# Performance work log

Hardware: AMD Instinct MI355X
Metric: run time of the kernel (lower is better)

The kernel has to match this reference:

```python
import jax, jax.numpy as jnp
import numpy as np

B, S, D = 2, 2048, 1024
H, DH = 16, 64  # num_heads, attention_dim


def setup_inputs() -> dict:
    key = jax.random.key(0)
    ks = jax.random.split(key, 10)
    x = jax.random.normal(ks[0], (B, S, D), dtype=jnp.float32)
    # causal mask, broadcast over batch and heads (mask==0 -> -inf)
    mask = jnp.tril(jnp.ones((S, S), dtype=jnp.int32))[None, None]
    s = 1.0 / np.sqrt(D)
    Wq = jax.random.normal(ks[1], (D, H * DH), dtype=jnp.float32) * s
    bq = jnp.zeros((H * DH,), dtype=jnp.float32)
    Wk = jax.random.normal(ks[2], (D, H * DH), dtype=jnp.float32) * s
    bk = jnp.zeros((H * DH,), dtype=jnp.float32)
    Wv = jax.random.normal(ks[3], (D, H * DH), dtype=jnp.float32) * s
    bv = jnp.zeros((H * DH,), dtype=jnp.float32)
    Wo = jax.random.normal(ks[4], (H * DH, D), dtype=jnp.float32) * (1.0 / np.sqrt(H * DH))
    bo = jnp.zeros((D,), dtype=jnp.float32)
    return {"x": x, "mask": mask, "Wq": Wq, "bq": bq, "Wk": Wk, "bk": bk,
            "Wv": Wv, "bv": bv, "Wo": Wo, "bo": bo}


def reference(x, mask, Wq, bq, Wk, bk, Wv, bv, Wo, bo):
    b, s, _ = x.shape
    q = (x @ Wq + bq).reshape(b, s, H, DH)
    k = (x @ Wk + bk).reshape(b, s, H, DH)
    v = (x @ Wv + bv).reshape(b, s, H, DH)
    # scores: [B, H, S, S]
    scores = jnp.einsum("bshd,bthd->bhst", q, k) / jnp.sqrt(jnp.float32(DH))
    scores = jnp.where(mask == 0, -jnp.inf, scores)
    w = jax.nn.softmax(scores, axis=-1)
    attended = jnp.einsum("bhst,bthd->bshd", w, v).reshape(b, s, H * DH)
    return attended @ Wo + bo
```

## Files before the change

### kernel.cpp

```cpp
#include <hip/hip_runtime.h>
#include <hip/hip_bf16.h>

#define B_ 2
#define S_ 2048
#define D_ 1024
#define H_ 16
#define DH_ 64

typedef __attribute__((ext_vector_type(8))) short bf16x8;
typedef __attribute__((ext_vector_type(4))) float f32x4;

#define QSCALE 0.18033688011112042f

__device__ __forceinline__ ushort f2b(float f){
  __hip_bfloat16 h = __float2bfloat16(f);
  return *reinterpret_cast<ushort*>(&h);
}

__device__ __forceinline__ unsigned cvtpk(float lo, float hi){
  unsigned r;
  asm("v_cvt_pk_bf16_f32 %0, %1, %2" : "=v"(r) : "v"(lo), "v"(hi));
  return r;
}

__device__ __forceinline__ void gload16(const ushort* g, ushort* l){
  __builtin_amdgcn_global_load_lds((const __attribute__((address_space(1))) unsigned*)g,
                                   (__attribute__((address_space(3))) unsigned*)l, 16, 0, 0);
}

__global__ __launch_bounds__(256) void k_prep(const float* __restrict__ x, ushort* __restrict__ xb,
                                              const float* __restrict__ Wq, const float* __restrict__ Wk,
                                              const float* __restrict__ Wv, const float* __restrict__ Wo,
                                              ushort* __restrict__ WqkvT, ushort* __restrict__ WoT){
  int bid = blockIdx.x, tid = threadIdx.x;
  if (bid < 2048){
    int i = (bid*256 + tid)*8;
    float4 v0 = *(const float4*)(x + i);
    float4 v1 = *(const float4*)(x + i + 4);
    uint4 o;
    o.x = f2b(v0.x) | ((unsigned)f2b(v0.y)<<16);
    o.y = f2b(v0.z) | ((unsigned)f2b(v0.w)<<16);
    o.z = f2b(v1.x) | ((unsigned)f2b(v1.y)<<16);
    o.w = f2b(v1.z) | ((unsigned)f2b(v1.w)<<16);
    *(uint4*)(xb + i) = o;
    return;
  }
  bid -= 2048;
  const int w = bid >> 10, tb = bid & 1023;
  const float* src = (w==0)?Wq:(w==1)?Wk:(w==2)?Wv:Wo;
  ushort* dst = (w==3)?WoT : WqkvT + (size_t)w*(1024*1024);
  __shared__ float tile[32][33];
  const int bx2 = tb & 31, by2 = tb >> 5;
  const int c0 = bx2*32, r0 = by2*32;
  const int tx = tid & 31, ty = tid >> 5;
  #pragma unroll
  for (int i=0;i<4;i++)
    tile[ty + i*8][tx] = src[(size_t)(r0 + ty + i*8)*1024 + c0 + tx];
  __syncthreads();
  #pragma unroll
  for (int i=0;i<4;i++)
    dst[(size_t)(c0 + ty + i*8)*1024 + r0 + tx] = f2b(tile[tx][ty + i*8]);
}

__global__ __launch_bounds__(512, 4) void k_gemm_qkv(const ushort* __restrict__ A,
                                                     const ushort* __restrict__ BT,
                                                     const float* __restrict__ b0p,
                                                     const float* __restrict__ b1p,
                                                     const float* __restrict__ b2p,
                                                     ushort* __restrict__ Cp,
                                                     int M, int N, int K){
  __shared__ ushort As[256*64];
  __shared__ ushort Bs[128*64];
  const int tid = threadIdx.x;
  const int nbn = N >> 7;
  const int bm = blockIdx.x / nbn, bn = blockIdx.x % nbn;
  const int m0 = bm << 8, n0 = bn << 7;
  const int wave = tid >> 6, lane = tid & 63;
  const int wm = (wave >> 1) << 6, wn = (wave & 1) << 6;
  const int lr = lane & 15, lq = lane >> 4;

  f32x4 acc[4][4] = {};

  const int r0 = tid >> 3;
  const int gk = (tid & 7) ^ (r0 & 7);
  const ushort* Agb = A  + (size_t)(m0 + r0)*K + gk*8;
  const ushort* Bgb = BT + (size_t)(n0 + r0)*K + gk*8;
  const int lofs = tid*8;

  for (int kt = 0; kt < K; kt += 64){
    __syncthreads();
    #pragma unroll
    for (int j=0;j<4;j++)
      gload16(Agb + (size_t)j*64*K + kt, &As[lofs + j*4096]);
    #pragma unroll
    for (int j=0;j<2;j++)
      gload16(Bgb + (size_t)j*64*K + kt, &Bs[lofs + j*4096]);
    __syncthreads();
    #pragma unroll
    for (int kk=0;kk<2;kk++){
      bf16x8 af[4], bfr[4];
      #pragma unroll
      for (int i=0;i<4;i++){
        int ra = wm + i*16 + lr;
        af[i]  = *(bf16x8*)&As[ra*64 + (((kk*4+lq) ^ (ra & 7)) << 3)];
        int rb = wn + i*16 + lr;
        bfr[i] = *(bf16x8*)&Bs[rb*64 + (((kk*4+lq) ^ (rb & 7)) << 3)];
      }
      __builtin_amdgcn_s_setprio(1);
      #pragma unroll
      for (int mi=0;mi<4;mi++)
        #pragma unroll
        for (int ni=0;ni<4;ni++)
          acc[mi][ni] = __builtin_amdgcn_mfma_f32_16x16x32_bf16(af[mi], bfr[ni], acc[mi][ni], 0, 0, 0);
      __builtin_amdgcn_s_setprio(0);
    }
  }

  const int seg = n0 >> 10;
  const float* bp = (seg==0 ? b0p : (seg==1 ? b1p : b2p));
  #pragma unroll
  for (int mi=0;mi<4;mi++){
    #pragma unroll
    for (int ni=0;ni<4;ni++){
      int col = n0 + wn + ni*16 + lr;
      int cl = col & 1023;
      float bv = bp[cl];
      int row0 = m0 + wm + mi*16 + lq*4;
      ushort* Qb = Cp;
      if (seg == 0){
        #pragma unroll
        for (int r=0;r<4;r++)
          Qb[(size_t)(row0+r)*1024 + cl] = f2b((acc[mi][ni][r] + bv) * QSCALE);
      } else if (seg == 1){
        ushort* Kb = Qb + (4u<<20);
        #pragma unroll
        for (int r=0;r<4;r++)
          Kb[(size_t)(row0+r)*1024 + cl] = f2b(acc[mi][ni][r] + bv);
      } else {
        ushort* Vt = Qb + (8u<<20);
        int bb = row0 >> 11, srow = row0 & 2047;
        uint2 pk;
        pk.x = cvtpk(acc[mi][ni][0]+bv, acc[mi][ni][1]+bv);
        pk.y = cvtpk(acc[mi][ni][2]+bv, acc[mi][ni][3]+bv);
        *(uint2*)&Vt[((size_t)(bb*1024 + cl))*2048 + srow] = pk;
      }
    }
  }
}

__global__ __launch_bounds__(256) void k_gemm_out(const ushort* __restrict__ A,
                                                  const ushort* __restrict__ BT,
                                                  const float* __restrict__ bias,
                                                  float* __restrict__ Cp,
                                                  int M, int N, int K){
  __shared__ ushort As[128*64];
  __shared__ ushort Bs[128*64];
  const int tid = threadIdx.x;
  const int nbn = N >> 7;
  const int bm = blockIdx.x / nbn, bn = blockIdx.x % nbn;
  const int m0 = bm << 7, n0 = bn << 7;
  const int wave = tid >> 6, lane = tid & 63;
  const int wm = (wave >> 1) << 6, wn = (wave & 1) << 6;
  const int lr = lane & 15, lq = lane >> 4;

  f32x4 acc[4][4] = {};

  const ushort* Ag[4]; const ushort* Bg[4]; int lofs[4];
  #pragma unroll
  for (int j=0;j<4;j++){
    int c = tid + j*256, row = c >> 3, slot = c & 7;
    int gk2 = slot ^ (row & 7);
    Ag[j] = A  + (size_t)(m0 + row)*K + gk2*8;
    Bg[j] = BT + (size_t)(n0 + row)*K + gk2*8;
    lofs[j] = c*8;
  }

  for (int kt = 0; kt < K; kt += 64){
    __syncthreads();
    #pragma unroll
    for (int j=0;j<4;j++){
      gload16(Ag[j] + kt, &As[lofs[j]]);
      gload16(Bg[j] + kt, &Bs[lofs[j]]);
    }
    __syncthreads();
    #pragma unroll
    for (int kk=0;kk<2;kk++){
      bf16x8 af[4], bfr[4];
      #pragma unroll
      for (int i=0;i<4;i++){
        int ra = wm + i*16 + lr;
        af[i]  = *(bf16x8*)&As[ra*64 + (((kk*4+lq) ^ (ra & 7)) << 3)];
        int rb = wn + i*16 + lr;
        bfr[i] = *(bf16x8*)&Bs[rb*64 + (((kk*4+lq) ^ (rb & 7)) << 3)];
      }
      __builtin_amdgcn_s_setprio(1);
      #pragma unroll
      for (int mi=0;mi<4;mi++)
        #pragma unroll
        for (int ni=0;ni<4;ni++)
          acc[mi][ni] = __builtin_amdgcn_mfma_f32_16x16x32_bf16(af[mi], bfr[ni], acc[mi][ni], 0, 0, 0);
      __builtin_amdgcn_s_setprio(0);
    }
  }

  #pragma unroll
  for (int mi=0;mi<4;mi++){
    #pragma unroll
    for (int ni=0;ni<4;ni++){
      int col = n0 + wn + ni*16 + lr;
      float bv = bias[col];
      int row0 = m0 + wm + mi*16 + lq*4;
      #pragma unroll
      for (int r=0;r<4;r++)
        Cp[(size_t)(row0+r)*N + col] = acc[mi][ni][r] + bv;
    }
  }
}

__device__ __forceinline__ bf16x8 lds_frag(const ushort* base, int row, int colbytes){
  return *(const bf16x8*)((const char*)base + row*128 + (colbytes ^ ((row & 7) << 4)));
}

__global__ __launch_bounds__(256) void k_attn_mfma(const ushort* __restrict__ Qb,
                                                   const ushort* __restrict__ Kb,
                                                   const ushort* __restrict__ Vtg,
                                                   ushort* __restrict__ Ob,
                                                   ushort* __restrict__ accPb,
                                                   float* __restrict__ lP){
  __shared__ ushort Ks[64*64];
  __shared__ ushort Vs[64*64];
  __shared__ ushort Ps[4][16*64];
  const int bid = blockIdx.x;
  int bh, qt, t0, NT, half; bool split;
  if (bid < 1024){
    int s = bid >> 5; bh = bid & 31;
    qt = 31 - (s >> 1); half = s & 1; split = true;
    if (half == 0){ t0 = 16; NT = qt; }
    else          { t0 = 0;  NT = 15; }
  } else {
    int s = bid - 1024; qt = 15 - (s >> 5); bh = s & 31;
    t0 = 0; NT = qt; half = 0; split = false;
  }
  const bool diag = (!split) || (half == 0);
  const int h = bh & 15, b = bh >> 4;
  const int q0 = qt << 6;
  const int tid = threadIdx.x;
  const int wq = tid >> 6, lane = tid & 63;
  const int ql = lane & 15, g = lane >> 4;

  bf16x8 Qf0, Qf1;
  {
    const ushort* qp = Qb + (size_t)(b*S_ + q0 + wq*16 + ql)*1024 + h*64 + g*8;
    Qf0 = *(const bf16x8*)(qp);
    Qf1 = *(const bf16x8*)(qp + 32);
  }
  bf16x8 ones;
  #pragma unroll
  for (int i=0;i<8;i++) ones[i] = (short)0x3F80;

  f32x4 lsum = {};
  f32x4 acc[4] = {};

  const int r0c = tid >> 3, cc = tid & 7;
  const int r1c = r0c + 32;
  const int ofs0 = r0c*128 + ((cc*16) ^ ((r0c & 7) << 4));
  const int ofs1 = r1c*128 + ((cc*16) ^ ((r1c & 7) << 4));
  const ushort* Kp0 = Kb  + (size_t)(b*S_ + r0c)*1024 + h*64 + cc*8;
  const ushort* Kp1 = Kb  + (size_t)(b*S_ + r1c)*1024 + h*64 + cc*8;
  const ushort* Vp0 = Vtg + (size_t)(bh*64 + r0c)*2048 + cc*8;
  const ushort* Vp1 = Vtg + (size_t)(bh*64 + r1c)*2048 + cc*8;

  uint4 ka, kc, va, vc;
  #define ALOAD(t) { \
    ka = *(const uint4*)(Kp0 + (size_t)(t)*65536); \
    kc = *(const uint4*)(Kp1 + (size_t)(t)*65536); \
    va = *(const uint4*)(Vp0 + (t)*64); \
    vc = *(const uint4*)(Vp1 + (t)*64); }

  char* Pb = (char*)Ps + wq*2048;

  ALOAD(t0);
  for (int kt = t0; ; ++kt){
    __syncthreads();
    *(uint4*)((char*)Ks + ofs0) = ka;
    *(uint4*)((char*)Ks + ofs1) = kc;
    *(uint4*)((char*)Vs + ofs0) = va;
    *(uint4*)((char*)Vs + ofs1) = vc;
    __syncthreads();
    if (kt < NT) ALOAD(kt+1);

    f32x4 sf[4] = {};
    __builtin_amdgcn_s_setprio(1);
    #pragma unroll
    for (int ki=0; ki<4; ++ki){
      bf16x8 kf = lds_frag(Ks, ki*16 + ql, g*16);
      sf[ki] = __builtin_amdgcn_mfma_f32_16x16x32_bf16(kf, Qf0, sf[ki], 0, 0, 0);
    }
    #pragma unroll
    for (int ki=0; ki<4; ++ki){
      bf16x8 kf = lds_frag(Ks, ki*16 + ql, 64 + g*16);
      sf[ki] = __builtin_amdgcn_mfma_f32_16x16x32_bf16(kf, Qf1, sf[ki], 0, 0, 0);
    }
    __builtin_amdgcn_s_setprio(0);

    float s[16];
    #pragma unroll
    for (int ki=0; ki<4; ++ki)
      #pragma unroll
      for (int r=0; r<4; ++r)
        s[ki*4+r] = sf[ki][r];
    if (diag && kt == NT){
      const int th = q0 + wq*16 + ql - NT*64;
      #pragma unroll
      for (int ki=0; ki<4; ++ki)
        #pragma unroll
        for (int r=0; r<4; ++r)
          if (ki*16 + g*4 + r > th) s[ki*4+r] = -1e30f;
    }
    #pragma unroll
    for (int i=0; i<16; ++i) s[i] = exp2f(s[i]);

    #pragma unroll
    for (int ki=0; ki<4; ++ki){
      uint2 uu;
      uu.x = cvtpk(s[ki*4+0], s[ki*4+1]);
      uu.y = cvtpk(s[ki*4+2], s[ki*4+3]);
      *(uint2*)(Pb + ql*128 + ((ki*32 + g*8) ^ ((ql & 7) << 4))) = uu;
    }

    __builtin_amdgcn_s_setprio(1);
    #pragma unroll
    for (int ks=0; ks<2; ++ks){
      bf16x8 pf = *(const bf16x8*)(Pb + ql*128 + ((ks*64 + g*16) ^ ((ql & 7) << 4)));
      #pragma unroll
      for (int ni=0; ni<4; ++ni){
        bf16x8 vf = lds_frag(Vs, ni*16 + ql, ks*64 + g*16);
        acc[ni] = __builtin_amdgcn_mfma_f32_16x16x32_bf16(pf, vf, acc[ni], 0, 0, 0);
      }
      lsum = __builtin_amdgcn_mfma_f32_16x16x32_bf16(pf, ones, lsum, 0, 0, 0);
    }
    __builtin_amdgcn_s_setprio(0);

    if (kt == NT) break;
  }
  #undef ALOAD

  if (!split){
    ushort* Op = Ob + (size_t)(b*S_ + q0 + wq*16)*1024 + h*64;
    #pragma unroll
    for (int r=0; r<4; ++r){
      float ir = 1.0f / lsum[r];
      #pragma unroll
      for (int ni=0; ni<4; ++ni)
        Op[(size_t)(g*4 + r)*1024 + ni*16 + ql] = f2b(acc[ni][r] * ir);
    }
  } else {
    const int slot = (qt - 16)*32 + bh;
    const int rbase = half*32768 + slot*64 + wq*16;
    #pragma unroll
    for (int r=0; r<4; ++r){
      const int tr = rbase + g*4 + r;
      float ir = 1.0f / lsum[r];
      #pragma unroll
      for (int ni=0; ni<4; ++ni)
        accPb[(size_t)tr*64 + ni*16 + ql] = f2b(acc[ni][r] * ir);
      if (ql == 0) lP[tr] = lsum[r];
    }
  }
}

__global__ __launch_bounds__(256) void k_combine(const ushort* __restrict__ accPb,
                                                 const float* __restrict__ lP,
                                                 ushort* __restrict__ Ob){
  const int slot = blockIdx.x;
  const int qt = 16 + (slot >> 5), bh = slot & 31;
  const int b = bh >> 4, h = bh & 15;
  const int row = threadIdx.x >> 2, dq = (threadIdx.x & 3) * 16;
  const int trA = slot*64 + row, trB = 32768 + slot*64 + row;
  float lA = lP[trA], lB = lP[trB];
  float inv = 1.0f / (lA + lB);
  float wA = lA * inv, wB = lB * inv;
  const ushort* pa = accPb + (size_t)trA*64 + dq;
  const ushort* pb = accPb + (size_t)trB*64 + dq;
  uint4 a0 = *(const uint4*)pa, a1 = *(const uint4*)(pa + 8);
  uint4 b0 = *(const uint4*)pb, b1 = *(const uint4*)(pb + 8);
  unsigned aw[8] = {a0.x,a0.y,a0.z,a0.w,a1.x,a1.y,a1.z,a1.w};
  unsigned bw[8] = {b0.x,b0.y,b0.z,b0.w,b1.x,b1.y,b1.z,b1.w};
  unsigned ow[8];
  #pragma unroll
  for (int e=0;e<8;e++){
    float alo = __uint_as_float(aw[e] << 16), ahi = __uint_as_float(aw[e] & 0xffff0000u);
    float blo = __uint_as_float(bw[e] << 16), bhi = __uint_as_float(bw[e] & 0xffff0000u);
    ow[e] = cvtpk(alo*wA + blo*wB, ahi*wA + bhi*wB);
  }
  ushort* op = Ob + (size_t)(b*S_ + qt*64 + row)*1024 + h*64 + dq;
  uint4 o0, o1;
  o0.x=ow[0]; o0.y=ow[1]; o0.z=ow[2]; o0.w=ow[3];
  o1.x=ow[4]; o1.y=ow[5]; o1.z=ow[6]; o1.w=ow[7];
  *(uint4*)(op)     = o0;
  *(uint4*)(op + 8) = o1;
}

extern "C" void kernel_launch(void* const* d_in, const int* in_sizes, int n_in,
                              void* d_out, int out_size, void* d_ws, size_t ws_size,
                              hipStream_t stream){
  const float* x  = (const float*)d_in[0];
  const float* Wq = (const float*)d_in[2];
  const float* bq = (const float*)d_in[3];
  const float* Wk = (const float*)d_in[4];
  const float* bk = (const float*)d_in[5];
  const float* Wv = (const float*)d_in[6];
  const float* bv = (const float*)d_in[7];
  const float* Wo = (const float*)d_in[8];
  const float* bo = (const float*)d_in[9];

  char* ws = (char*)d_ws;
  const size_t MB = 1024u*1024u;
  ushort* xb    = (ushort*)(ws + 0);
  ushort* WqkvT = (ushort*)(ws + 8*MB);
  ushort* WoT   = (ushort*)(ws + 14*MB);
  ushort* Qb    = (ushort*)(ws + 16*MB);
  ushort* Kb    = (ushort*)(ws + 24*MB);
  ushort* Vtg   = (ushort*)(ws + 32*MB);
  float*  lP    = (float*)(ws + 40*MB);
  ushort* attb  = xb;
  ushort* accPb = (ushort*)d_out;

  const int MN = B_*S_;

  k_prep<<<dim3(6144), dim3(256), 0, stream>>>(x, xb, Wq, Wk, Wv, Wo, WqkvT, WoT);

  k_gemm_qkv<<<dim3((MN/256)*(3072/128)), dim3(512), 0, stream>>>(xb, WqkvT, bq, bk, bv, Qb, MN, 3072, 1024);

  k_attn_mfma<<<dim3(1536), dim3(256), 0, stream>>>(Qb, Kb, Vtg, attb, accPb, lP);
  k_combine<<<dim3(512), dim3(256), 0, stream>>>(accPb, lP, attb);

  k_gemm_out<<<dim3((MN/128)*(1024/128)), dim3(256), 0, stream>>>(attb, WoT, bo, (float*)d_out, MN, 1024, 1024);
}
```

Baseline: 112.5 us.

## Split attention KV range into fixed ten-tile chunks with multi-way combine

The attention work split changes from a two-way split for the upper half of query tiles to chunks of at most ten KV tiles, giving 1 to 4 chunks per query tile and 2176 blocks. The combine kernel now merges a variable number of partial results per row, weighted by their row sums. The aim is to even out per-block work and shorten the tail of the causal attention launch. In exchange it adds more partial-result traffic and a larger combine pass.

Measured after the change: 113.1 us. No clear change (+0.5%).

```diff
diff --git a/kernel.cpp b/kernel.cpp
--- a/kernel.cpp
+++ b/kernel.cpp
@@ -11,6 +11,11 @@
 typedef __attribute__((ext_vector_type(4))) float f32x4;
 
 #define QSCALE 0.18033688011112042f
+
+__device__ __forceinline__ int chunk_off(int qt){
+  return (qt <= 19) ? 2*(qt-10) : (qt <= 29 ? 20 + 3*(qt-20) : 50 + 4*(qt-30));
+}
+#define CHUNKS_PER_BH 58
 
 __device__ __forceinline__ ushort f2b(float f){
   __hip_bfloat16 h = __float2bfloat16(f);
@@ -231,17 +236,17 @@
   __shared__ ushort Vs[64*64];
   __shared__ ushort Ps[4][16*64];
   const int bid = blockIdx.x;
-  int bh, qt, t0, NT, half; bool split;
-  if (bid < 1024){
-    int s = bid >> 5; bh = bid & 31;
-    qt = 31 - (s >> 1); half = s & 1; split = true;
-    if (half == 0){ t0 = 16; NT = qt; }
-    else          { t0 = 0;  NT = 15; }
-  } else {
-    int s = bid - 1024; qt = 15 - (s >> 5); bh = s & 31;
-    t0 = 0; NT = qt; half = 0; split = false;
-  }
-  const bool diag = (!split) || (half == 0);
+  const int bh = bid & 31;
+  const int j = 67 - (bid >> 5);
+  int qt, c, nc;
+  if (j < 10)      { qt = j;                c = 0;              nc = 1; }
+  else if (j < 30) { int t = j-10; qt = 10 + (t>>1); c = t & 1; nc = 2; }
+  else if (j < 60) { int t = j-30; int q3 = t/3; qt = 20 + q3; c = t - 3*q3; nc = 3; }
+  else             { int t = j-60; qt = 30 + (t>>2); c = t & 3; nc = 4; }
+  const int t0 = c*10;
+  const int NT = min(t0 + 9, qt);
+  const bool diag = (NT == qt);
+  const bool split = (nc > 1);
   const int h = bh & 15, b = bh >> 4;
   const int q0 = qt << 6;
   const int tid = threadIdx.x;
@@ -355,8 +360,7 @@
         Op[(size_t)(g*4 + r)*1024 + ni*16 + ql] = f2b(acc[ni][r] * ir);
     }
   } else {
-    const int slot = (qt - 16)*32 + bh;
-    const int rbase = half*32768 + slot*64 + wq*16;
+    const int rbase = (bh*CHUNKS_PER_BH + chunk_off(qt) + c)*64 + wq*16;
     #pragma unroll
     for (int r=0; r<4; ++r){
       const int tr = rbase + g*4 + r;
@@ -372,27 +376,35 @@
 __global__ __launch_bounds__(256) void k_combine(const ushort* __restrict__ accPb,
                                                  const float* __restrict__ lP,
                                                  ushort* __restrict__ Ob){
-  const int slot = blockIdx.x;
-  const int qt = 16 + (slot >> 5), bh = slot & 31;
+  const int bid = blockIdx.x;
+  const int qt = 10 + (bid >> 5), bh = bid & 31;
   const int b = bh >> 4, h = bh & 15;
+  const int nc = (qt <= 19) ? 2 : (qt <= 29 ? 3 : 4);
+  const int base = bh*CHUNKS_PER_BH + chunk_off(qt);
   const int row = threadIdx.x >> 2, dq = (threadIdx.x & 3) * 16;
-  const int trA = slot*64 + row, trB = 32768 + slot*64 + row;
-  float lA = lP[trA], lB = lP[trB];
-  float inv = 1.0f / (lA + lB);
-  float wA = lA * inv, wB = lB * inv;
-  const ushort* pa = accPb + (size_t)trA*64 + dq;
-  const ushort* pb = accPb + (size_t)trB*64 + dq;
-  uint4 a0 = *(const uint4*)pa, a1 = *(const uint4*)(pa + 8);
-  uint4 b0 = *(const uint4*)pb, b1 = *(const uint4*)(pb + 8);
-  unsigned aw[8] = {a0.x,a0.y,a0.z,a0.w,a1.x,a1.y,a1.z,a1.w};
-  unsigned bw[8] = {b0.x,b0.y,b0.z,b0.w,b1.x,b1.y,b1.z,b1.w};
+
+  float w[4];
+  float lt = 0.f;
+  for (int i=0;i<nc;++i){ w[i] = lP[(base+i)*64 + row]; lt += w[i]; }
+  float inv = 1.0f / lt;
+
+  float o[16];
+  #pragma unroll
+  for (int e=0;e<16;++e) o[e] = 0.f;
+  for (int i=0;i<nc;++i){
+    float wi = w[i] * inv;
+    const ushort* p = accPb + (size_t)((base+i)*64 + row)*64 + dq;
+    uint4 a0 = *(const uint4*)p, a1 = *(const uint4*)(p + 8);
+    unsigned aw[8] = {a0.x,a0.y,a0.z,a0.w,a1.x,a1.y,a1.z,a1.w};
+    #pragma unroll
+    for (int e=0;e<8;++e){
+      o[e*2]   += wi * __uint_as_float(aw[e] << 16);
+      o[e*2+1] += wi * __uint_as_float(aw[e] & 0xffff0000u);
+    }
+  }
   unsigned ow[8];
   #pragma unroll
-  for (int e=0;e<8;e++){
-    float alo = __uint_as_float(aw[e] << 16), ahi = __uint_as_float(aw[e] & 0xffff0000u);
-    float blo = __uint_as_float(bw[e] << 16), bhi = __uint_as_float(bw[e] & 0xffff0000u);
-    ow[e] = cvtpk(alo*wA + blo*wB, ahi*wA + bhi*wB);
-  }
+  for (int e=0;e<8;++e) ow[e] = cvtpk(o[e*2], o[e*2+1]);
   ushort* op = Ob + (size_t)(b*S_ + qt*64 + row)*1024 + h*64 + dq;
   uint4 o0, o1;
   o0.x=ow[0]; o0.y=ow[1]; o0.z=ow[2]; o0.w=ow[3];
@@ -432,8 +444,8 @@
 
   k_gemm_qkv<<<dim3((MN/256)*(3072/128)), dim3(512), 0, stream>>>(xb, WqkvT, bq, bk, bv, Qb, MN, 3072, 1024);
 
-  k_attn_mfma<<<dim3(1536), dim3(256), 0, stream>>>(Qb, Kb, Vtg, attb, accPb, lP);
-  k_combine<<<dim3(512), dim3(256), 0, stream>>>(accPb, lP, attb);
+  k_attn_mfma<<<dim3(2176), dim3(256), 0, stream>>>(Qb, Kb, Vtg, attb, accPb, lP);
+  k_combine<<<dim3(704), dim3(256), 0, stream>>>(accPb, lP, attb);
 
   k_gemm_out<<<dim3((MN/128)*(1024/128)), dim3(256), 0, stream>>>(attb, WoT, bo, (float*)d_out, MN, 1024, 1024);
 }
```
